# Optimization experiments

Measured on AMD Instinct MI355X. Metric: run time of the kernel, lower is better.

Reference implementation:

```python
import jax, jax.numpy as jnp
import numpy as np

NUM_POINTS = 200_000
AMBIENT_DIM = 3
NUM_THETAS = 128
RESOLUTION = 128
BATCH_SIZE = 64


def setup_inputs() -> dict:
    key = jax.random.key(0)
    kx, kv, kb = jax.random.split(key, 3)
    x = jax.random.normal(kx, (NUM_POINTS, AMBIENT_DIM), dtype=jnp.float32)
    # unit-norm direction vectors, columns of v [ambient_dim, num_thetas]
    v = jax.random.normal(kv, (AMBIENT_DIM, NUM_THETAS), dtype=jnp.float32)
    v = v / jnp.linalg.norm(v, axis=0, keepdims=True)
    batch = jnp.sort(jax.random.randint(kb, (NUM_POINTS,), 0, BATCH_SIZE, dtype=jnp.int32))
    return {"x": x, "v": v, "batch": batch, "resolution": RESOLUTION, "batch_size": BATCH_SIZE}


def reference(x, v, batch, resolution, batch_size):
    # projected heights: [N, T]
    nh = x @ v
    N, T = nh.shape
    # bin heights over the unit ball [-1, 1] into `resolution` bins (fast ECT bincount)
    bins = jnp.clip(jnp.floor((nh + 1.0) * (0.5 * resolution)).astype(jnp.int32), 0, resolution - 1)
    theta = jnp.arange(T, dtype=jnp.int32)  # [T]
    # flat scatter index over (batch, bin, theta)
    flat = (batch.astype(jnp.int32)[:, None] * resolution + bins) * T + theta[None, :]
    hist = jnp.zeros((batch_size * resolution * T,), dtype=x.dtype)
    hist = hist.at[flat.reshape(-1)].add(1.0)
    hist = hist.reshape(batch_size, resolution, T)
    # cumulative histogram along the filtration (resolution) axis = ECT
    ect = jnp.cumsum(hist, axis=1)  # [B, resolution, num_thetas]
    return ect
```

## Files before the change

kernel.cpp:

```cpp
#include <hip/hip_runtime.h>


constexpr int N_PTS    = 200000;
constexpr int T        = 128;
constexpr int R        = 128;
constexpr int B        = 64;
constexpr int SPLIT_T  = 4;
constexpr int TT       = T / SPLIT_T;
constexpr int NTHREADS = 1024;
constexpr int TG       = 8;
constexpr int PL       = NTHREADS / TG;
constexpr int UNROLL   = 4;
constexpr int SUBS     = NTHREADS / TT;
constexpr int RCH      = R / SUBS;

__device__ __forceinline__ int lower_bound_i32(const int* __restrict__ a, int n, int val) {
    int lo = 0, hi = n;
    while (lo < hi) {
        int mid = (lo + hi) >> 1;
        if (a[mid] < val) lo = mid + 1; else hi = mid;
    }
    return lo;
}

__global__ __launch_bounds__(NTHREADS)
void FastEctLayer_73065983639654_kernel(const float* __restrict__ x,
                                        const float* __restrict__ v,
                                        const int*   __restrict__ batch,
                                        float*       __restrict__ out) {
    __shared__ unsigned int hist[R * TT];
    __shared__ unsigned int partial[SUBS * TT];

    const int tid    = threadIdx.x;
    const int tg     = tid & (TG - 1);
    const int pl     = tid >> 3;
    const int bat    = blockIdx.x / SPLIT_T;
    const int theta0 = (blockIdx.x % SPLIT_T) * TT;

    for (int i = tid; i < R * TT; i += NTHREADS) hist[i] = 0u;

    int   tlj[4];
    float vv0[4], vv1[4], vv2[4];
#pragma unroll
    for (int j = 0; j < 4; ++j) {
        const int tl = (4 * tg + j + pl) & (TT - 1);
        tlj[j] = tl;
        vv0[j] = v[0 * T + theta0 + tl];
        vv1[j] = v[1 * T + theta0 + tl];
        vv2[j] = v[2 * T + theta0 + tl];
    }

    const int start = lower_bound_i32(batch, N_PTS, bat);
    const int end   = lower_bound_i32(batch, N_PTS, bat + 1);

    __syncthreads();

    int p = start + pl;
    for (; p + (UNROLL - 1) * PL < end; p += UNROLL * PL) {
        float c0[UNROLL], c1[UNROLL], c2[UNROLL];
#pragma unroll
        for (int u = 0; u < UNROLL; ++u) {
            const int q = p + u * PL;
            c0[u] = x[q * 3 + 0];
            c1[u] = x[q * 3 + 1];
            c2[u] = x[q * 3 + 2];
        }
#pragma unroll
        for (int u = 0; u < UNROLL; ++u) {
#pragma unroll
            for (int j = 0; j < 4; ++j) {
                const float nh = fmaf(c0[u], vv0[j], fmaf(c1[u], vv1[j], c2[u] * vv2[j]));
                int bin = (int)fmaf(nh, 0.5f * (float)R, 0.5f * (float)R);
                bin = min(max(bin, 0), R - 1);
                atomicAdd(&hist[bin * TT + tlj[j]], 1u);
            }
        }
    }
    for (; p < end; p += PL) {
        const float x0 = x[p * 3 + 0], x1 = x[p * 3 + 1], x2 = x[p * 3 + 2];
#pragma unroll
        for (int j = 0; j < 4; ++j) {
            const float nh = fmaf(x0, vv0[j], fmaf(x1, vv1[j], x2 * vv2[j]));
            int bin = (int)fmaf(nh, 0.5f * (float)R, 0.5f * (float)R);
            bin = min(max(bin, 0), R - 1);
            atomicAdd(&hist[bin * TT + tlj[j]], 1u);
        }
    }

    __syncthreads();

    const int tl  = tid & (TT - 1);
    const int sub = tid / TT;
    const int r0  = sub * RCH;
    unsigned int csum = 0;
#pragma unroll
    for (int r = r0; r < r0 + RCH; ++r) csum += hist[r * TT + tl];
    partial[sub * TT + tl] = csum;
    __syncthreads();

    unsigned int run = 0;
    for (int s = 0; s < sub; ++s) run += partial[s * TT + tl];
#pragma unroll
    for (int r = r0; r < r0 + RCH; ++r) {
        run += hist[r * TT + tl];
        out[((size_t)bat * R + r) * T + theta0 + tl] = (float)run;
    }
}

extern "C" void kernel_launch(void* const* d_in, const int* in_sizes, int n_in,
                              void* d_out, int out_size, void* d_ws, size_t ws_size,
                              hipStream_t stream) {
    const float* x     = (const float*)d_in[0];
    const float* v     = (const float*)d_in[1];
    const int*   batch = (const int*)d_in[2];
    float*       out   = (float*)d_out;

    dim3 grid(B * SPLIT_T);
    dim3 block(NTHREADS);
    hipLaunchKernelGGL(FastEctLayer_73065983639654_kernel, grid, block, 0, stream,
                       x, v, batch, out);
}
```

Measured before the change: 77.32 us.

## Use wave-parallel ballot search for batch bounds and float4 point loads

Replaces the per-thread serial binary search over the batch array with a 64-way search in one wave per bound, using ballot and popcount, and shares the result through shared memory. The point loop now reads four points at a time as three float4 loads, aligned down to a multiple of four, with boundary checks for partial chunks. This aims to cut redundant global loads and search latency, and to widen point loads. The cost is extra branching at chunk edges and more register use.

```diff
diff --git a/kernel.cpp b/kernel.cpp
--- a/kernel.cpp
+++ b/kernel.cpp
@@ -10,18 +10,8 @@
 constexpr int NTHREADS = 1024;
 constexpr int TG       = 8;
 constexpr int PL       = NTHREADS / TG;
-constexpr int UNROLL   = 4;
 constexpr int SUBS     = NTHREADS / TT;
 constexpr int RCH      = R / SUBS;
-
-__device__ __forceinline__ int lower_bound_i32(const int* __restrict__ a, int n, int val) {
-    int lo = 0, hi = n;
-    while (lo < hi) {
-        int mid = (lo + hi) >> 1;
-        if (a[mid] < val) lo = mid + 1; else hi = mid;
-    }
-    return lo;
-}
 
 __global__ __launch_bounds__(NTHREADS)
 void FastEctLayer_73065983639654_kernel(const float* __restrict__ x,
@@ -30,6 +20,7 @@
                                         float*       __restrict__ out) {
     __shared__ unsigned int hist[R * TT];
     __shared__ unsigned int partial[SUBS * TT];
+    __shared__ int s_range[2];
 
     const int tid    = threadIdx.x;
     const int tg     = tid & (TG - 1);
@@ -38,6 +29,27 @@
     const int theta0 = (blockIdx.x % SPLIT_T) * TT;
 
     for (int i = tid; i < R * TT; i += NTHREADS) hist[i] = 0u;
+
+    const int wave = tid >> 6, lane = tid & 63;
+    if (wave < 2) {
+        const int val = bat + wave;
+        int lo = 0, hi = N_PTS;
+        while (lo < hi) {
+            const int step = (hi - lo + 63) >> 6;
+            const int pos  = lo + lane * step;
+            const bool pred = (pos < hi) && (batch[pos] < val);
+            const unsigned long long m = __ballot(pred);
+            const int k = __popcll(m);
+            if (k == 0) {
+                hi = lo;
+            } else {
+                const int nlo = lo + (k - 1) * step + 1;
+                hi = min(hi, lo + k * step);
+                lo = nlo;
+            }
+        }
+        if (lane == 0) s_range[wave] = lo;
+    }
 
     int   tlj[4];
     float vv0[4], vv1[4], vv2[4];
@@ -50,41 +62,58 @@
         vv2[j] = v[2 * T + theta0 + tl];
     }
 
-    const int start = lower_bound_i32(batch, N_PTS, bat);
-    const int end   = lower_bound_i32(batch, N_PTS, bat + 1);
+    __syncthreads();
+    const int start = s_range[0];
+    const int end   = s_range[1];
 
-    __syncthreads();
+    const int a0      = start & ~3;
+    const int nchunks = (end - a0 + 3) >> 2;
+    const float4* __restrict__ X4 = (const float4*)x;
+    const int cbase = (a0 >> 2) * 3;
 
-    int p = start + pl;
-    for (; p + (UNROLL - 1) * PL < end; p += UNROLL * PL) {
-        float c0[UNROLL], c1[UNROLL], c2[UNROLL];
+    auto process4 = [&](int pbase, float4 f0, float4 f1, float4 f2) {
+        const float px[4] = {f0.x, f0.w, f1.z, f2.y};
+        const float py[4] = {f0.y, f1.x, f1.w, f2.z};
+        const float pz[4] = {f0.z, f1.y, f2.x, f2.w};
+        if (pbase >= start && pbase + 3 < end) {
 #pragma unroll
-        for (int u = 0; u < UNROLL; ++u) {
-            const int q = p + u * PL;
-            c0[u] = x[q * 3 + 0];
-            c1[u] = x[q * 3 + 1];
-            c2[u] = x[q * 3 + 2];
-        }
+            for (int i = 0; i < 4; ++i) {
 #pragma unroll
-        for (int u = 0; u < UNROLL; ++u) {
+                for (int j = 0; j < 4; ++j) {
+                    const float nh = fmaf(px[i], vv0[j], fmaf(py[i], vv1[j], pz[i] * vv2[j]));
+                    int bin = (int)fmaf(nh, 0.5f * (float)R, 0.5f * (float)R);
+                    bin = min(max(bin, 0), R - 1);
+                    atomicAdd(&hist[bin * TT + tlj[j]], 1u);
+                }
+            }
+        } else {
 #pragma unroll
-            for (int j = 0; j < 4; ++j) {
-                const float nh = fmaf(c0[u], vv0[j], fmaf(c1[u], vv1[j], c2[u] * vv2[j]));
-                int bin = (int)fmaf(nh, 0.5f * (float)R, 0.5f * (float)R);
-                bin = min(max(bin, 0), R - 1);
-                atomicAdd(&hist[bin * TT + tlj[j]], 1u);
+            for (int i = 0; i < 4; ++i) {
+                const int p = pbase + i;
+                if (p >= start && p < end) {
+#pragma unroll
+                    for (int j = 0; j < 4; ++j) {
+                        const float nh = fmaf(px[i], vv0[j], fmaf(py[i], vv1[j], pz[i] * vv2[j]));
+                        int bin = (int)fmaf(nh, 0.5f * (float)R, 0.5f * (float)R);
+                        bin = min(max(bin, 0), R - 1);
+                        atomicAdd(&hist[bin * TT + tlj[j]], 1u);
+                    }
+                }
             }
         }
+    };
+
+    int c = pl;
+    for (; c + PL < nchunks; c += 2 * PL) {
+        const int c2 = c + PL;
+        const float4 fa0 = X4[cbase + 3 * c],  fa1 = X4[cbase + 3 * c + 1],  fa2 = X4[cbase + 3 * c + 2];
+        const float4 fb0 = X4[cbase + 3 * c2], fb1 = X4[cbase + 3 * c2 + 1], fb2 = X4[cbase + 3 * c2 + 2];
+        process4(a0 + 4 * c,  fa0, fa1, fa2);
+        process4(a0 + 4 * c2, fb0, fb1, fb2);
     }
-    for (; p < end; p += PL) {
-        const float x0 = x[p * 3 + 0], x1 = x[p * 3 + 1], x2 = x[p * 3 + 2];
-#pragma unroll
-        for (int j = 0; j < 4; ++j) {
-            const float nh = fmaf(x0, vv0[j], fmaf(x1, vv1[j], x2 * vv2[j]));
-            int bin = (int)fmaf(nh, 0.5f * (float)R, 0.5f * (float)R);
-            bin = min(max(bin, 0), R - 1);
-            atomicAdd(&hist[bin * TT + tlj[j]], 1u);
-        }
+    for (; c < nchunks; c += PL) {
+        const float4 f0 = X4[cbase + 3 * c], f1 = X4[cbase + 3 * c + 1], f2 = X4[cbase + 3 * c + 2];
+        process4(a0 + 4 * c, f0, f1, f2);
     }
 
     __syncthreads();
```

Measured after the change: 71.82 us. 7.1% less time.
